# Kernel optimization log

Measured on AMD Instinct MI355X. Metric: run time of the kernel, lower is better.

Reference implementation:

```python
import jax, jax.numpy as jnp
import numpy as np

N_HEAD = 8
HID = 256
V_DIM = HID // N_HEAD
NQ = 2048
NK = 2048
BATCH = 16
LOCALITY = 50.0  # percentile threshold; <=100 enables local masking


def setup_inputs() -> dict:
    key = jax.random.key(0)
    k1, k2, k3, k4 = jax.random.split(key, 4)
    m_dist = jax.random.uniform(k1, (N_HEAD, NQ, NK), dtype=jnp.float32)
    x = jax.random.normal(k2, (BATCH, NK, HID), dtype=jnp.float32)
    r = jax.random.normal(k3, (N_HEAD, 1, 1), dtype=jnp.float32)
    weight = jax.random.normal(k4, (N_HEAD, HID, V_DIM), dtype=jnp.float32) / jnp.sqrt(
        jnp.float32(HID)
    )
    return {"m_dist": m_dist, "x": x, "r": r, "weight": weight}


def reference(m_dist, x, r, weight):
    # distance scaling: tan(pi/4 * (1-eps) * (1 + sin(r))), per head
    scale = jnp.tan(0.25 * jnp.pi * (1.0 - 1e-07) * (1.0 + jnp.sin(r)))  # [H,1,1]
    scaled = m_dist * scale  # [H, Nq, Nk]
    # percentile-threshold local masking per (head, query) row
    thr = jnp.percentile(scaled, LOCALITY, axis=-1, keepdims=True)  # [H, Nq, 1]
    scaled = jnp.where(scaled <= thr, scaled, jnp.inf)
    att = jax.nn.softmax(-scaled, axis=-1)  # [H, Nq, Nk]
    value = jnp.einsum("bnj,hjk->bhnk", x, weight)  # [B, H, Nk, v]
    out = jnp.einsum("hjn,bhnk->bhjk", att, value)  # [B, H, Nq, v]
    out = jnp.transpose(out, (0, 2, 1, 3)).reshape(out.shape[0], out.shape[2], -1)
    return jax.nn.gelu(out)  # [B, Nq, HID]
```

## Files before the change

kernel.cpp:

```cpp
#include <hip/hip_runtime.h>
#include <hip/hip_bf16.h>

#define NH   8
#define HID  256
#define VD   32
#define NQ   2048
#define NKK  2048
#define NB   16
#define NN   512

typedef short bf16x8 __attribute__((ext_vector_type(8)));
typedef float f32x4 __attribute__((ext_vector_type(4)));

__device__ inline unsigned short f2bf(float f) {
  unsigned int u = __float_as_uint(f);
  u += 0x7FFFu + ((u >> 16) & 1u);
  return (unsigned short)(u >> 16);
}

__device__ inline void gload_lds16(const void* g, void* l) {
  __builtin_amdgcn_global_load_lds(
      (const __attribute__((address_space(1))) void*)g,
      (__attribute__((address_space(3))) void*)l, 16, 0, 0);
}

__device__ inline float gelu_f(float x) {
  float u2 = 1.5957691216057308f * (x + 0.044715f * x * x * x);
  float e = __expf(u2);
  return 0.5f * x * (1.0f + (e - 1.0f) / (e + 1.0f));
}


__global__ __launch_bounds__(256) void wt_kernel(
    const float* __restrict__ w, unsigned short* __restrict__ wT) {
  const int n = blockIdx.x;
  const int j = threadIdx.x;
  wT[(size_t)n * HID + j] = f2bf(w[(size_t)(n >> 5) * HID * VD + (size_t)j * VD + (n & 31)]);
}

__global__ __launch_bounds__(256) void value_kernel(
    const unsigned short* __restrict__ wT, const float* __restrict__ x,
    unsigned short* __restrict__ vT) {
  const int hvt = blockIdx.x & 1;
  const int kt  = blockIdx.x >> 1;
  const int b   = blockIdx.y;
  const int m0 = hvt * 128;
  const int n0 = kt * 128;
  const int t = threadIdx.x;
  const int lane = t & 63, wid = t >> 6;
  const int wr = wid >> 1, wc = wid & 1;

  __shared__ __align__(16) unsigned short As[128 * 32];
  __shared__ __align__(16) unsigned short Bs[128 * 32];

  const int rowL = t >> 2;
  const int cb = (((t & 3) ^ ((t >> 3) & 3)) * 8);
  const unsigned short* gA0 = wT + (size_t)(m0 + rowL) * HID + cb;
  const unsigned short* gA1 = gA0 + (size_t)64 * HID;
  char* lA0 = (char*)As + t * 16;
  char* lA1 = (char*)As + 4096 + t * 16;

  const int brow = t >> 1, bj = (t & 1) * 16;
  const float* gB = x + ((size_t)b * NKK + n0 + brow) * HID + bj;
  const int bc = (brow >> 1) & 3;
  const int bs0 = (2 * (t & 1)) ^ bc;
  unsigned short* lB0 = Bs + brow * 32 + bs0 * 8;
  unsigned short* lB1 = Bs + brow * 32 + (bs0 ^ 1) * 8;

  f32x4 acc[4][4];
#pragma unroll
  for (int i = 0; i < 4; ++i)
#pragma unroll
    for (int j = 0; j < 4; ++j) acc[i][j] = (f32x4){0.f, 0.f, 0.f, 0.f};

  const int fr = lane & 15;
  const int kb = (((lane >> 4) ^ ((fr >> 1) & 3)) * 16);
  const char* baseA = (const char*)As + (wr * 64 + fr) * 64 + kb;
  const char* baseB = (const char*)Bs + (wc * 64 + fr) * 64 + kb;

  f32x4 p0 = *(const f32x4*)(gB + 0);
  f32x4 p1 = *(const f32x4*)(gB + 4);
  f32x4 p2 = *(const f32x4*)(gB + 8);
  f32x4 p3 = *(const f32x4*)(gB + 12);

  for (int kk = 0; kk < HID / 32; ++kk) {
    gload_lds16(gA0, lA0);
    gload_lds16(gA1, lA1);
    gA0 += 32; gA1 += 32;

    f32x4 c0 = p0, c1 = p1, c2 = p2, c3 = p3;
    if (kk < HID / 32 - 1) {
      const float* nb = gB + (kk + 1) * 32;
      p0 = *(const f32x4*)(nb + 0);
      p1 = *(const f32x4*)(nb + 4);
      p2 = *(const f32x4*)(nb + 8);
      p3 = *(const f32x4*)(nb + 12);
    }
    uint4 pk0, pk1;
    pk0.x = (unsigned)f2bf(c0[0]) | ((unsigned)f2bf(c0[1]) << 16);
    pk0.y = (unsigned)f2bf(c0[2]) | ((unsigned)f2bf(c0[3]) << 16);
    pk0.z = (unsigned)f2bf(c1[0]) | ((unsigned)f2bf(c1[1]) << 16);
    pk0.w = (unsigned)f2bf(c1[2]) | ((unsigned)f2bf(c1[3]) << 16);
    pk1.x = (unsigned)f2bf(c2[0]) | ((unsigned)f2bf(c2[1]) << 16);
    pk1.y = (unsigned)f2bf(c2[2]) | ((unsigned)f2bf(c2[3]) << 16);
    pk1.z = (unsigned)f2bf(c3[0]) | ((unsigned)f2bf(c3[1]) << 16);
    pk1.w = (unsigned)f2bf(c3[2]) | ((unsigned)f2bf(c3[3]) << 16);
    *(uint4*)lB0 = pk0;
    *(uint4*)lB1 = pk1;

    __syncthreads();

    bf16x8 a[4], bfr[4];
#pragma unroll
    for (int i = 0; i < 4; ++i) a[i] = *(const bf16x8*)(baseA + i * 16 * 64);
#pragma unroll
    for (int j = 0; j < 4; ++j) bfr[j] = *(const bf16x8*)(baseB + j * 16 * 64);
#pragma unroll
    for (int i = 0; i < 4; ++i)
#pragma unroll
      for (int j = 0; j < 4; ++j)
        acc[i][j] = __builtin_amdgcn_mfma_f32_16x16x32_bf16(a[i], bfr[j], acc[i][j], 0, 0, 0);
    __syncthreads();
  }

  const int hvb = m0 + wr * 64 + (lane >> 4) * 4;
  const int kc0 = n0 + wc * 64 + (lane & 15);
#pragma unroll
  for (int i = 0; i < 4; ++i) {
#pragma unroll
    for (int j = 0; j < 4; ++j) {
      int kc = kc0 + j * 16;
#pragma unroll
      for (int e = 0; e < 4; ++e) {
        int hv = hvb + i * 16 + e;
        int h = hv >> 5, v = hv & 31;
        vT[((size_t)h * NN + b * VD + v) * NKK + kc] = f2bf(acc[i][j][e]);
      }
    }
  }
}

__global__ __launch_bounds__(256) void att_kernel(
    const float* __restrict__ m_dist, const float* __restrict__ r,
    unsigned short* __restrict__ att) {
  const int w = threadIdx.x >> 6;
  const int lane = threadIdx.x & 63;
  const int row = (blockIdx.x << 2) | w;
  const int h = row >> 11;

  __shared__ unsigned int histS[4][256];
  __shared__ float collS[4][160];
  __shared__ unsigned int cntS[4];
  __shared__ float vabS[4][2];

  unsigned int* hist = histS[w];
  float* coll = collS[w];

  const float C = (float)(0.25 * 3.141592653589793 * (1.0 - 1e-7));
  float sc = tanf(C * (1.0f + sinf(r[h])));

  *(uint4*)&hist[lane * 4] = (uint4){0u, 0u, 0u, 0u};
  if (lane == 0) cntS[w] = 0u;

  const float* md = m_dist + (size_t)row * NKK;
  f32x4 m4[8];
#pragma unroll
  for (int k = 0; k < 8; ++k) m4[k] = *(const f32x4*)(md + 4 * lane + 256 * k);

  float mn = 1e30f;
#pragma unroll
  for (int k = 0; k < 8; ++k)
#pragma unroll
    for (int e = 0; e < 4; ++e) {
      float v = m4[k][e];
      mn = fminf(mn, v);
      int bin = min(max((int)(v * 256.0f), 0), 255);
      atomicAdd(&hist[bin], 1u);
    }
#pragma unroll
  for (int off = 32; off; off >>= 1) mn = fminf(mn, __shfl_xor(mn, off));

  asm volatile("s_waitcnt lgkmcnt(0)" ::: "memory");
  uint4 hc = *(const uint4*)&hist[lane * 4];
  unsigned c0 = hc.x, c1 = hc.x + hc.y, c2 = c1 + hc.z, c3 = c2 + hc.w;
  unsigned g = c3;
  unsigned incl = g;
#pragma unroll
  for (int off = 1; off < 64; off <<= 1) {
    unsigned y = __shfl_up(incl, off);
    if (lane >= off) incl += y;
  }
  unsigned excl = incl - g;

  unsigned long long ba1 = __ballot(incl >= 1024u);
  int glA = __ffsll((unsigned long long)ba1) - 1;
  unsigned eA = __shfl(excl, glA);
  unsigned a0 = __shfl(excl + c0, glA), a1 = __shfl(excl + c1, glA), a2 = __shfl(excl + c2, glA);
  int bA; unsigned below;
  if (a0 >= 1024u)      { bA = glA * 4 + 0; below = eA; }
  else if (a1 >= 1024u) { bA = glA * 4 + 1; below = a0; }
  else if (a2 >= 1024u) { bA = glA * 4 + 2; below = a1; }
  else                  { bA = glA * 4 + 3; below = a2; }
  unsigned long long ba2 = __ballot(incl >= 1025u);
  int glB = __ffsll((unsigned long long)ba2) - 1;
  unsigned e0 = __shfl(excl + c0, glB), e1 = __shfl(excl + c1, glB), e2 = __shfl(excl + c2, glB);
  int bB = (e0 >= 1025u) ? glB * 4 : (e1 >= 1025u) ? glB * 4 + 1
                                   : (e2 >= 1025u) ? glB * 4 + 2 : glB * 4 + 3;

#pragma unroll
  for (int k = 0; k < 8; ++k)
#pragma unroll
    for (int e = 0; e < 4; ++e) {
      float v = m4[k][e];
      int bin = min(max((int)(v * 256.0f), 0), 255);
      if (bin >= bA && bin <= bB) {
        unsigned idx = atomicAdd(&cntS[w], 1u);
        if (idx < 160u) coll[idx] = v;
      }
    }
  asm volatile("s_waitcnt lgkmcnt(0)" ::: "memory");
  const int n = (int)min(cntS[w], 160u);
  const int ra = 1023 - (int)below, rb = 1024 - (int)below;
#pragma unroll
  for (int e2 = 0; e2 < 3; ++e2) {
    int idx = lane + (e2 << 6);
    if (idx < n) {
      float v = coll[idx];
      int rank = 0;
      for (int j2 = 0; j2 < n; ++j2) {
        float u = coll[j2];
        rank += (u < v || (u == v && j2 < idx)) ? 1 : 0;
      }
      if (rank == ra) vabS[w][0] = v;
      if (rank == rb) vabS[w][1] = v;
    }
  }
  asm volatile("s_waitcnt lgkmcnt(0)" ::: "memory");
  float thr = 0.5f * (vabS[w][0] * sc) + 0.5f * (vabS[w][1] * sc);
  float minscaled = mn * sc;

  float wsum = 0.f;
#pragma unroll
  for (int k = 0; k < 8; ++k)
#pragma unroll
    for (int e = 0; e < 4; ++e) {
      float s = m4[k][e] * sc;
      float ev = (s <= thr) ? __expf(minscaled - s) : 0.f;
      m4[k][e] = ev;
      wsum += ev;
    }
#pragma unroll
  for (int off = 32; off; off >>= 1) wsum += __shfl_xor(wsum, off);
  float inv = 1.0f / wsum;

  unsigned short* ao = att + (size_t)row * NKK;
#pragma unroll
  for (int k = 0; k < 8; ++k) {
    uint2 pk;
    pk.x = (unsigned)f2bf(m4[k][0] * inv) | ((unsigned)f2bf(m4[k][1] * inv) << 16);
    pk.y = (unsigned)f2bf(m4[k][2] * inv) | ((unsigned)f2bf(m4[k][3] * inv) << 16);
    *(uint2*)(ao + 4 * lane + 256 * k) = pk;
  }
}

__global__ __launch_bounds__(256) void gemm_kernel(
    const unsigned short* __restrict__ att, const unsigned short* __restrict__ vT,
    float* __restrict__ out) {
  const int bid = blockIdx.x;
  const int h = bid & 7;
  const int tile = bid >> 3;
  const int qt = tile >> 2, nt = tile & 3;
  const int q0 = qt * 128, n0 = nt * 128;
  const int t = threadIdx.x;
  const int lane = t & 63, wid = t >> 6;
  const int wr = wid >> 1, wc = wid & 1;

  __shared__ __align__(16) unsigned short As[4][128 * 32];
  __shared__ __align__(16) unsigned short Bs[4][128 * 32];

  const int rowL = t >> 2;
  const int cb = (((t & 3) ^ ((t >> 3) & 3)) * 8);

  const unsigned short* gA = att + ((size_t)h * NQ + q0 + rowL) * NKK + cb;
  const unsigned short* gB = vT + ((size_t)h * NN + n0 + rowL) * NKK + cb;
  const int ldsOff = t * 16;

#define STAGE(BI, KT) do {                                                  \
    const unsigned short* a_ = gA + (KT) * 32;                              \
    const unsigned short* b_ = gB + (KT) * 32;                              \
    char* lA_ = (char*)As[(BI)] + ldsOff;                                   \
    char* lB_ = (char*)Bs[(BI)] + ldsOff;                                   \
    gload_lds16(a_, lA_);                                                   \
    gload_lds16(a_ + (size_t)64 * NKK, lA_ + 4096);                         \
    gload_lds16(b_, lB_);                                                   \
    gload_lds16(b_ + (size_t)64 * NKK, lB_ + 4096);                         \
  } while (0)

  f32x4 acc[4][4];
#pragma unroll
  for (int i = 0; i < 4; ++i)
#pragma unroll
    for (int j = 0; j < 4; ++j) acc[i][j] = (f32x4){0.f, 0.f, 0.f, 0.f};

  const int fr = lane & 15;
  const int kb = (((lane >> 4) ^ ((fr >> 1) & 3)) * 16);
  const int fragOff = (wr * 64 + fr) * 64 + kb;
  const int fragOffB = (wc * 64 + fr) * 64 + kb;

  STAGE(0, 0);
  STAGE(1, 1);
  STAGE(2, 2);
  asm volatile("s_waitcnt vmcnt(8)\n\ts_barrier" ::: "memory");

  for (int kt = 0; kt < 64; kt += 4) {
#pragma unroll
    for (int u = 0; u < 4; ++u) {
      const char* bA = (const char*)As[u] + fragOff;
      const char* bB = (const char*)Bs[u] + fragOffB;
      bf16x8 a[4], b[4];
#pragma unroll
      for (int i = 0; i < 4; ++i) a[i] = *(const bf16x8*)(bA + i * 1024);
#pragma unroll
      for (int j = 0; j < 4; ++j) b[j] = *(const bf16x8*)(bB + j * 1024);
      STAGE((u + 3) & 3, (kt + u + 3) & 63);
      __builtin_amdgcn_s_setprio(1);
#pragma unroll
      for (int i = 0; i < 4; ++i)
#pragma unroll
        for (int j = 0; j < 4; ++j)
          acc[i][j] = __builtin_amdgcn_mfma_f32_16x16x32_bf16(a[i], b[j], acc[i][j], 0, 0, 0);
      __builtin_amdgcn_s_setprio(0);
      asm volatile("s_waitcnt vmcnt(8)\n\ts_barrier" ::: "memory");
    }
  }
  asm volatile("s_waitcnt vmcnt(0)" ::: "memory");
#undef STAGE

  const int orow = q0 + wr * 64 + (lane >> 4) * 4;
  const int ocol0 = n0 + wc * 64 + (lane & 15);
#pragma unroll
  for (int i = 0; i < 4; ++i) {
#pragma unroll
    for (int j = 0; j < 4; ++j) {
      int ncol = ocol0 + j * 16;
      int bb = ncol >> 5, vv = ncol & 31;
      float* op = out + ((size_t)bb * NQ + orow + i * 16) * HID + h * VD + vv;
#pragma unroll
      for (int e = 0; e < 4; ++e) op[(size_t)e * HID] = gelu_f(acc[i][j][e]);
    }
  }
}

extern "C" void kernel_launch(void* const* d_in, const int* in_sizes, int n_in,
                              void* d_out, int out_size, void* d_ws, size_t ws_size,
                              hipStream_t stream) {
  const float* m_dist = (const float*)d_in[0];
  const float* x      = (const float*)d_in[1];
  const float* r      = (const float*)d_in[2];
  const float* weight = (const float*)d_in[3];
  float* out = (float*)d_out;

  unsigned short* att = (unsigned short*)d_ws;
  unsigned short* vT  = (unsigned short*)((char*)d_ws + (size_t)NH * NQ * NKK * 2);
  unsigned short* wT  = (unsigned short*)((char*)d_ws + (size_t)NH * NQ * NKK * 2 +
                                          (size_t)NH * NN * NKK * 2);

  wt_kernel<<<dim3(256), dim3(256), 0, stream>>>(weight, wT);
  value_kernel<<<dim3(32, NB), dim3(256), 0, stream>>>(wT, x, vT);
  att_kernel<<<dim3(NH * NQ / 4), dim3(256), 0, stream>>>(m_dist, r, att);
  gemm_kernel<<<dim3(NH * 64), dim3(256), 0, stream>>>(att, vT, out);
}
```

Measured before the change: 103.7 us.

## Fuse weight transpose into value kernel and tune attention threshold kernel

Removes the separate weight-transpose kernel: the value GEMM now loads fp32 weight columns directly with strided reads, converts them to bf16 and writes them swizzled into LDS. This saves one launch and a workspace round trip, at the cost of uncoalesced per-element weight loads inside the GEMM loop. The att_kernel gets an occupancy hint of 8 blocks per CU and padded shared histogram/collection arrays. Its percentile candidate buffer grows to 192 entries, with the rank loop rewritten as a stride loop.

```diff
diff --git a/kernel.cpp b/kernel.cpp
--- a/kernel.cpp
+++ b/kernel.cpp
@@ -31,19 +31,13 @@
 }
 
 
-__global__ __launch_bounds__(256) void wt_kernel(
-    const float* __restrict__ w, unsigned short* __restrict__ wT) {
-  const int n = blockIdx.x;
-  const int j = threadIdx.x;
-  wT[(size_t)n * HID + j] = f2bf(w[(size_t)(n >> 5) * HID * VD + (size_t)j * VD + (n & 31)]);
-}
-
 __global__ __launch_bounds__(256) void value_kernel(
-    const unsigned short* __restrict__ wT, const float* __restrict__ x,
+    const float* __restrict__ w, const float* __restrict__ x,
     unsigned short* __restrict__ vT) {
-  const int hvt = blockIdx.x & 1;
-  const int kt  = blockIdx.x >> 1;
-  const int b   = blockIdx.y;
+  const int vb  = blockIdx.x;
+  const int hvt = vb & 1;
+  const int kt  = (vb >> 1) & 15;
+  const int b   = vb >> 5;
   const int m0 = hvt * 128;
   const int n0 = kt * 128;
   const int t = threadIdx.x;
@@ -53,12 +47,13 @@
   __shared__ __align__(16) unsigned short As[128 * 32];
   __shared__ __align__(16) unsigned short Bs[128 * 32];
 
-  const int rowL = t >> 2;
-  const int cb = (((t & 3) ^ ((t >> 3) & 3)) * 8);
-  const unsigned short* gA0 = wT + (size_t)(m0 + rowL) * HID + cb;
-  const unsigned short* gA1 = gA0 + (size_t)64 * HID;
-  char* lA0 = (char*)As + t * 16;
-  char* lA1 = (char*)As + 4096 + t * 16;
+  const int arow = t >> 1;
+  const int ahalf = t & 1;
+  const int hh = (m0 + arow) >> 5, avv = (m0 + arow) & 31;
+  const float* wbase = w + ((size_t)hh * HID + ahalf * 16) * VD + avv;
+  const int ac = (arow >> 1) & 3;
+  unsigned short* wA0 = (unsigned short*)((char*)As + arow * 64 + (((2 * ahalf) ^ ac) * 16));
+  unsigned short* wA1 = (unsigned short*)((char*)As + arow * 64 + (((2 * ahalf + 1) ^ ac) * 16));
 
   const int brow = t >> 1, bj = (t & 1) * 16;
   const float* gB = x + ((size_t)b * NKK + n0 + brow) * HID + bj;
@@ -84,9 +79,9 @@
   f32x4 p3 = *(const f32x4*)(gB + 12);
 
   for (int kk = 0; kk < HID / 32; ++kk) {
-    gload_lds16(gA0, lA0);
-    gload_lds16(gA1, lA1);
-    gA0 += 32; gA1 += 32;
+    float av[16];
+#pragma unroll
+    for (int e = 0; e < 16; ++e) av[e] = wbase[((size_t)kk * 32 + e) * VD];
 
     f32x4 c0 = p0, c1 = p1, c2 = p2, c3 = p3;
     if (kk < HID / 32 - 1) {
@@ -96,6 +91,18 @@
       p2 = *(const f32x4*)(nb + 8);
       p3 = *(const f32x4*)(nb + 12);
     }
+    uint4 qa0, qa1;
+    qa0.x = (unsigned)f2bf(av[0]) | ((unsigned)f2bf(av[1]) << 16);
+    qa0.y = (unsigned)f2bf(av[2]) | ((unsigned)f2bf(av[3]) << 16);
+    qa0.z = (unsigned)f2bf(av[4]) | ((unsigned)f2bf(av[5]) << 16);
+    qa0.w = (unsigned)f2bf(av[6]) | ((unsigned)f2bf(av[7]) << 16);
+    qa1.x = (unsigned)f2bf(av[8]) | ((unsigned)f2bf(av[9]) << 16);
+    qa1.y = (unsigned)f2bf(av[10]) | ((unsigned)f2bf(av[11]) << 16);
+    qa1.z = (unsigned)f2bf(av[12]) | ((unsigned)f2bf(av[13]) << 16);
+    qa1.w = (unsigned)f2bf(av[14]) | ((unsigned)f2bf(av[15]) << 16);
+    *(uint4*)wA0 = qa0;
+    *(uint4*)wA1 = qa1;
+
     uint4 pk0, pk1;
     pk0.x = (unsigned)f2bf(c0[0]) | ((unsigned)f2bf(c0[1]) << 16);
     pk0.y = (unsigned)f2bf(c0[2]) | ((unsigned)f2bf(c0[3]) << 16);
@@ -140,7 +147,7 @@
   }
 }
 
-__global__ __launch_bounds__(256) void att_kernel(
+__global__ __launch_bounds__(256, 8) void att_kernel(
     const float* __restrict__ m_dist, const float* __restrict__ r,
     unsigned short* __restrict__ att) {
   const int w = threadIdx.x >> 6;
@@ -148,8 +155,8 @@
   const int row = (blockIdx.x << 2) | w;
   const int h = row >> 11;
 
-  __shared__ unsigned int histS[4][256];
-  __shared__ float collS[4][160];
+  __shared__ unsigned int histS[4][257];
+  __shared__ float collS[4][193];
   __shared__ unsigned int cntS[4];
   __shared__ float vabS[4][2];
 
@@ -215,25 +222,21 @@
       int bin = min(max((int)(v * 256.0f), 0), 255);
       if (bin >= bA && bin <= bB) {
         unsigned idx = atomicAdd(&cntS[w], 1u);
-        if (idx < 160u) coll[idx] = v;
+        if (idx < 192u) coll[idx] = v;
       }
     }
   asm volatile("s_waitcnt lgkmcnt(0)" ::: "memory");
-  const int n = (int)min(cntS[w], 160u);
+  const int n = (int)min(cntS[w], 192u);
   const int ra = 1023 - (int)below, rb = 1024 - (int)below;
-#pragma unroll
-  for (int e2 = 0; e2 < 3; ++e2) {
-    int idx = lane + (e2 << 6);
-    if (idx < n) {
-      float v = coll[idx];
-      int rank = 0;
-      for (int j2 = 0; j2 < n; ++j2) {
-        float u = coll[j2];
-        rank += (u < v || (u == v && j2 < idx)) ? 1 : 0;
-      }
-      if (rank == ra) vabS[w][0] = v;
-      if (rank == rb) vabS[w][1] = v;
-    }
+  for (int idx = lane; idx < n; idx += 64) {
+    float v = coll[idx];
+    int rank = 0;
+    for (int j2 = 0; j2 < n; ++j2) {
+      float u = coll[j2];
+      rank += (u < v || (u == v && j2 < idx)) ? 1 : 0;
+    }
+    if (rank == ra) vabS[w][0] = v;
+    if (rank == rb) vabS[w][1] = v;
   }
   asm volatile("s_waitcnt lgkmcnt(0)" ::: "memory");
   float thr = 0.5f * (vabS[w][0] * sc) + 0.5f * (vabS[w][1] * sc);
@@ -362,11 +365,8 @@
 
   unsigned short* att = (unsigned short*)d_ws;
   unsigned short* vT  = (unsigned short*)((char*)d_ws + (size_t)NH * NQ * NKK * 2);
-  unsigned short* wT  = (unsigned short*)((char*)d_ws + (size_t)NH * NQ * NKK * 2 +
-                                          (size_t)NH * NN * NKK * 2);
-
-  wt_kernel<<<dim3(256), dim3(256), 0, stream>>>(weight, wT);
-  value_kernel<<<dim3(32, NB), dim3(256), 0, stream>>>(wT, x, vT);
+
+  value_kernel<<<dim3(512), dim3(256), 0, stream>>>(weight, x, vT);
   att_kernel<<<dim3(NH * NQ / 4), dim3(256), 0, stream>>>(m_dist, r, att);
   gemm_kernel<<<dim3(NH * 64), dim3(256), 0, stream>>>(att, vT, out);
 }
```

Result: slower. 143.6 us (+38.4%).
